# Kernel optimization log

Measured on AMD Instinct MI355X. Metric: run time of the kernel, lower is better.

The kernel has to match this reference:

```python
import jax, jax.numpy as jnp
import numpy as np

NUM_HEADS = 4
LN_EPS = 1e-5


def setup_inputs() -> dict:
    key = jax.random.key(0)
    ks = jax.random.split(key, 12)
    B, S, D = 8, 2048, 256
    Dh = D // NUM_HEADS
    s = 0.02
    return {
        "descriptors": jax.random.normal(ks[0], (B, S, D), jnp.float32),
        # cached rotary embedding (cos, sin) pair broadcastable over heads
        "keypoints": jax.random.normal(ks[1], (2, B, 1, S, Dh), jnp.float32),
        "Wqkv_w": jax.random.normal(ks[2], (3 * D, D), jnp.float32) * s,
        "Wqkv_b": jax.random.normal(ks[3], (3 * D,), jnp.float32) * s,
        "Wo_w": jax.random.normal(ks[4], (D, D), jnp.float32) * s,
        "Wo_b": jax.random.normal(ks[5], (D,), jnp.float32) * s,
        "W1_w": jax.random.normal(ks[6], (2 * D, 2 * D), jnp.float32) * s,
        "W1_b": jax.random.normal(ks[7], (2 * D,), jnp.float32) * s,
        "ln_g": jnp.ones((2 * D,), jnp.float32),
        "ln_b": jnp.zeros((2 * D,), jnp.float32),
        "W2_w": jax.random.normal(ks[8], (D, 2 * D), jnp.float32) * s,
        "W2_b": jax.random.normal(ks[9], (D,), jnp.float32) * s,
    }


def _rotate_half(x):
    # pairwise rotation: (x0,x1,x2,x3,...) -> (-x1,x0,-x3,x2,...)
    xr = x.reshape(x.shape[:-1] + (x.shape[-1] // 2, 2))
    return jnp.stack((-xr[..., 1], xr[..., 0]), axis=-1).reshape(x.shape)


def reference(descriptors, keypoints, Wqkv_w, Wqkv_b, Wo_w, Wo_b,
              W1_w, W1_b, ln_g, ln_b, W2_w, W2_b):
    B, S, D = descriptors.shape
    H = NUM_HEADS
    Dh = D // H
    # fused QKV projection; torch layout: last dim = (H, Dh, 3) interleaved
    qkv = descriptors @ Wqkv_w.T + Wqkv_b           # [B,S,3D]
    qkv = qkv.reshape(B, S, H, Dh, 3).transpose(0, 2, 1, 3, 4)  # [B,H,S,Dh,3]
    q, k, v = qkv[..., 0], qkv[..., 1], qkv[..., 2]
    # rotary embedding on q, k
    cos, sin = keypoints[0], keypoints[1]           # [B,1,S,Dh]
    q = q * cos + _rotate_half(q) * sin
    k = k * cos + _rotate_half(k) * sin
    # scaled dot-product attention
    scale = jnp.float32(Dh) ** -0.5
    sim = jnp.einsum('bhid,bhjd->bhij', q, k) * scale
    attn = jax.nn.softmax(sim, axis=-1)
    ctx = jnp.einsum('bhij,bhjd->bhid', attn, v)    # [B,H,S,Dh]
    ctx = ctx.transpose(0, 2, 1, 3).reshape(B, S, D)
    message = ctx @ Wo_w.T + Wo_b
    # FFN over concat(descriptors, message)
    x = jnp.concatenate([descriptors, message], axis=-1)  # [B,S,2D]
    x = x @ W1_w.T + W1_b
    mu = jnp.mean(x, axis=-1, keepdims=True)
    var = jnp.var(x, axis=-1, keepdims=True)
    x = (x - mu) * jax.lax.rsqrt(var + LN_EPS) * ln_g + ln_b
    x = jax.nn.gelu(x, approximate=False)
    x = x @ W2_w.T + W2_b
    return descriptors + x
```

## Files before the change

### kernel.cpp

```cpp
#include <hip/hip_runtime.h>
#include <math.h>

#define B_  8
#define S_  2048
#define D_  256
#define H_  4
#define DH  64
#define M_  (B_ * S_)
#define QS  4194304

typedef __attribute__((ext_vector_type(8))) short bf16x8;
typedef __attribute__((ext_vector_type(4))) float f32x4;
typedef unsigned short u16;
typedef unsigned int   u32;

#define AS1 __attribute__((address_space(1)))
#define AS3 __attribute__((address_space(3)))

__device__ __forceinline__ u16 f2bf(float x) {
    union { float f; u32 u; } c; c.f = x;
    u32 r = (c.u + 0x7fffu + ((c.u >> 16) & 1u)) >> 16;
    return (u16)r;
}
__device__ __forceinline__ float bf2f(u16 x) {
    union { u32 u; float f; } c; c.u = ((u32)x) << 16;
    return c.f;
}

__device__ __forceinline__ void gload16(const void* g, void* l) {
    __builtin_amdgcn_global_load_lds((const AS1 unsigned int*)g,
                                     (AS3 unsigned int*)l, 16, 0, 0);
}

__global__ __launch_bounds__(256) void cast7_kernel(
    const float* __restrict__ desc, u16* __restrict__ descb,
    const float* __restrict__ wqkv, u16* __restrict__ wqkvb,
    const float* __restrict__ wo,   const float* __restrict__ w1,
    u16* __restrict__ w1f,
    const float* __restrict__ w2,   u16* __restrict__ w2b,
    const float* __restrict__ w1_b, const float* __restrict__ wo_b,
    float* __restrict__ bias1f)
{
    int bid = blockIdx.x;
    const int tid = threadIdx.x;

    if (bid >= 5184) {
        const int row = bid - 5184;
        const int col = tid;
        const float* wrow = w1 + (size_t)row * 512 + 256;
        float acc = 0.f;
#pragma unroll 4
        for (int k = 0; k < 256; k++)
            acc += wrow[k] * wo[(size_t)k * 256 + col];
        w1f[(size_t)row * 512 + 256 + col] = f2bf(acc);
        return;
    }
    if (bid >= 4672) {
        __shared__ float red[4];
        const int n = bid - 4672;
        float p = w1[(size_t)n * 512 + 256 + tid] * wo_b[tid];
#pragma unroll
        for (int off = 1; off < 64; off <<= 1) p += __shfl_xor(p, off);
        if ((tid & 63) == 0) red[tid >> 6] = p;
        __syncthreads();
        if (tid == 0) bias1f[n] = red[0] + red[1] + red[2] + red[3] + w1_b[n];
        return;
    }
    if (bid >= 4544) {
        const int i = ((bid - 4544) * 256 + tid) * 4;
        const float4 v = *(const float4*)(w2 + i);
        u16 o[4] = {f2bf(v.x), f2bf(v.y), f2bf(v.z), f2bf(v.w)};
        *(uint2*)(w2b + i) = *(const uint2*)o;
        return;
    }
    if (bid >= 4288) {
        const int e = ((bid - 4288) * 256 + tid) * 4;
        const int row = e >> 9, col = e & 511;
        if (col < 256) {
            const float4 v = *(const float4*)(w1 + e);
            u16 o[4] = {f2bf(v.x), f2bf(v.y), f2bf(v.z), f2bf(v.w)};
            *(uint2*)(w1f + (size_t)row * 512 + col) = *(const uint2*)o;
        }
        return;
    }
    const float* s; u16* d;
    if (bid < 4096) { s = desc; d = descb; }
    else            { s = wqkv; d = wqkvb; bid -= 4096; }
    const int i = (bid * 256 + tid) * 4;
    const float4 v = *(const float4*)(s + i);
    u16 o[4] = {f2bf(v.x), f2bf(v.y), f2bf(v.z), f2bf(v.w)};
    *(uint2*)(d + i) = *(const uint2*)o;
}

template <int NT, int CONCAT, int RES, int OUTBF16>
__global__ __launch_bounds__(256) void gemm_bf16(
    const u16* __restrict__ A, const u16* __restrict__ A2,
    const u16* __restrict__ W, const float* __restrict__ bias,
    const float* __restrict__ res, float* __restrict__ Cf,
    u16* __restrict__ Cb, int K, int N, int ldc)
{
    __shared__ u16 As[128 * 64];
    __shared__ u16 Bs[NT * 32 * 64];
    const int tid  = threadIdx.x;
    const int w    = tid >> 6;
    const int lane = tid & 63;
    const int n    = lane & 15;
    const int quad = lane >> 4;
    const int m0   = blockIdx.x * 128;
    const int n0   = blockIdx.y * (NT * 32);
    const int m_off = (w >> 1) * 64;
    const int n_off = (w & 1) * (NT * 16);
    const int lrow = lane >> 3;
    const int lcol = (lane & 7) * 8;

    f32x4 acc[4][NT];
#pragma unroll
    for (int i = 0; i < 4; i++)
#pragma unroll
        for (int j = 0; j < NT; j++) acc[i][j] = (f32x4){0.f, 0.f, 0.f, 0.f};

    for (int k0 = 0; k0 < K; k0 += 64) {
        const u16* Asrc;
        int kb, lda;
        if (CONCAT) { Asrc = (k0 < 256) ? A : A2; kb = k0 & 255; lda = 256; }
        else        { Asrc = A; kb = k0; lda = K; }

        __syncthreads();
#pragma unroll
        for (int it = 0; it < 4; it++) {
            const int r0 = it * 32 + w * 8;
            gload16(Asrc + (size_t)(m0 + r0 + lrow) * lda + kb + lcol, &As[r0 * 64]);
        }
#pragma unroll
        for (int it = 0; it < NT; it++) {
            const int r0 = it * 32 + w * 8;
            gload16(W + (size_t)(n0 + r0 + lrow) * K + k0 + lcol, &Bs[r0 * 64]);
        }
        __syncthreads();

        bf16x8 af[4][2], bf[NT][2];
#pragma unroll
        for (int mt = 0; mt < 4; mt++)
#pragma unroll
            for (int t = 0; t < 2; t++)
                af[mt][t] = *(const bf16x8*)&As[(m_off + mt * 16 + n) * 64 + t * 32 + quad * 8];
#pragma unroll
        for (int nt = 0; nt < NT; nt++)
#pragma unroll
            for (int t = 0; t < 2; t++)
                bf[nt][t] = *(const bf16x8*)&Bs[(n_off + nt * 16 + n) * 64 + t * 32 + quad * 8];

#pragma unroll
        for (int mt = 0; mt < 4; mt++)
#pragma unroll
            for (int nt = 0; nt < NT; nt++) {
                acc[mt][nt] = __builtin_amdgcn_mfma_f32_16x16x32_bf16(af[mt][0], bf[nt][0], acc[mt][nt], 0, 0, 0);
                acc[mt][nt] = __builtin_amdgcn_mfma_f32_16x16x32_bf16(af[mt][1], bf[nt][1], acc[mt][nt], 0, 0, 0);
            }
    }

#pragma unroll
    for (int nt = 0; nt < NT; nt++) {
        const int col = n0 + n_off + nt * 16 + n;
        const float bv = bias[col];
#pragma unroll
        for (int mt = 0; mt < 4; mt++) {
#pragma unroll
            for (int r = 0; r < 4; r++) {
                const int row = m0 + m_off + mt * 16 + quad * 4 + r;
                float o = acc[mt][nt][r] + bv;
                if (RES) o += res[(size_t)row * ldc + col];
                if (OUTBF16) Cb[(size_t)row * ldc + col] = f2bf(o);
                else         Cf[(size_t)row * ldc + col] = o;
            }
        }
    }
}

#define QSCALE 0.18033688011112042f

__global__ __launch_bounds__(256) void ropevt_kernel(
    const u16* __restrict__ qkv, const float* __restrict__ kp,
    u16* __restrict__ q, u16* __restrict__ k, u16* __restrict__ vt)
{
    __shared__ u32 vbuf[32 * 128];

    const int bh = blockIdx.x;
    const int s0 = blockIdx.y * 128;
    const int b  = bh >> 2;
    const int h  = bh & 3;
    const int t  = threadIdx.x;
    const int dp = t & 31;
    const int d  = dp * 2;

    const size_t qkbase = ((size_t)bh * S_ + s0) * DH;
#pragma unroll
    for (int i = 0; i < 16; i++) {
        const int sl = i * 8 + (t >> 5);
        const int s  = s0 + sl;
        const u16* src = qkv + (size_t)(b * S_ + s) * 768 + h * 192 + dp * 6;
        const u32 w0 = *(const u32*)(src);
        const u32 w1 = *(const u32*)(src + 2);
        const u32 w2 = *(const u32*)(src + 4);
        const float qe = bf2f((u16)w0), ke = bf2f((u16)(w0 >> 16));
        const float qo = bf2f((u16)(w1 >> 16));
        const float ko = bf2f((u16)w2);

        const size_t kidx = ((size_t)b * S_ + s) * DH + d;
        const float2 cs = *(const float2*)(kp + kidx);
        const float2 sn = *(const float2*)(kp + (size_t)B_ * S_ * DH + kidx);

        const float qe2 = (qe * cs.x - qo * sn.x) * QSCALE;
        const float qo2 = (qo * cs.y + qe * sn.y) * QSCALE;
        const float ke2 = ke * cs.x - ko * sn.x;
        const float ko2 = ko * cs.y + ke * sn.y;

        const size_t oidx = qkbase + (size_t)sl * DH + d;
        *(u32*)(q + oidx) = (u32)f2bf(qe2) | ((u32)f2bf(qo2) << 16);
        *(u32*)(k + oidx) = (u32)f2bf(ke2) | ((u32)f2bf(ko2) << 16);
        vbuf[dp * 128 + (sl ^ dp)] = (w1 & 0xffffu) | (w2 & 0xffff0000u);
    }
    __syncthreads();

    u16* vtp = vt + (size_t)bh * DH * S_ + s0;
#pragma unroll
    for (int i = 0; i < 16; i++) {
        const int dd  = i * 4 + (t >> 6);
        const int sp  = t & 63;
        const int dpr = dd >> 1;
        const u32 a = vbuf[dpr * 128 + ((2 * sp)     ^ dpr)];
        const u32 c = vbuf[dpr * 128 + ((2 * sp + 1) ^ dpr)];
        const u32 o = (dd & 1) ? ((a >> 16)      | (c & 0xffff0000u))
                               : ((a & 0xffffu)  | (c << 16));
        *(u32*)(vtp + (size_t)dd * S_ + 2 * sp) = o;
    }
}

#define NEG12L2E -17.312340490667562f

__global__ __launch_bounds__(256, 2) void attn_kernel(
    const u16* __restrict__ q, const u16* __restrict__ k,
    const u16* __restrict__ vt, u16* __restrict__ ctx)
{
    __shared__ u16 ks[128 * 64];
    __shared__ u16 qs[128 * 64];
    __shared__ u16 vs[64 * 128];
    __shared__ u16 ps[128 * 128];

    const int tid  = threadIdx.x;
    const int w    = tid >> 6;
    const int lane = tid & 63;
    const int n    = lane & 15;
    const int quad = lane >> 4;
    const int lrow = lane >> 3;
    const int vrow = lane >> 4;
    const int bh   = blockIdx.x;
    const int q0   = blockIdx.y * 128;
    const int b    = bh >> 2;
    const int h    = bh & 3;
    const int nsw  = n & 7;

    const int kcol  = (((lane & 7) ^ lrow) * 8);
    const int vcol0 = (((lane & 15) ^ vrow) * 8);
    const int vcol1 = (((lane & 15) ^ (4 + vrow)) * 8);

    const u16* qbase = q  + (size_t)bh * S_ * DH;
    const u16* kbase = k  + (size_t)bh * S_ * DH;
    const u16* vbase = vt + (size_t)bh * DH * S_;

#pragma unroll
    for (int it = 0; it < 4; it++) {
        const int idx = it * 256 + tid;
        const int row = idx >> 3;
        const int c8  = idx & 7;
        *(uint4*)&qs[row * 64 + ((c8 ^ (row & 7)) * 8)] =
            *(const uint4*)(qbase + (size_t)(q0 + row) * DH + c8 * 8);
    }
    __syncthreads();

    bf16x8 qf[2][2];
#pragma unroll
    for (int mb = 0; mb < 2; mb++) {
        qf[mb][0] = *(const bf16x8*)&qs[(w * 32 + mb * 16 + n) * 64 + ((quad       ^ nsw) * 8)];
        qf[mb][1] = *(const bf16x8*)&qs[(w * 32 + mb * 16 + n) * 64 + (((4 + quad) ^ nsw) * 8)];
    }

    f32x4 o[2][4];
#pragma unroll
    for (int mb = 0; mb < 2; mb++)
#pragma unroll
        for (int j = 0; j < 4; j++) o[mb][j] = (f32x4){0.f, 0.f, 0.f, 0.f};
    float lrun[2] = {0.f, 0.f};

    for (int kb = 0; kb < S_ / 128; kb++) {
        const int k0 = kb * 128;
        __syncthreads();
#pragma unroll
        for (int it = 0; it < 4; it++) {
            const int r0 = w * 32 + it * 8;
            gload16(kbase + (size_t)(k0 + r0 + lrow) * DH + kcol, &ks[r0 * 64]);
            const int d0 = w * 16 + it * 4;
            gload16(vbase + (size_t)(d0 + vrow) * S_ + k0 + ((it & 1) ? vcol1 : vcol0),
                    &vs[d0 * 128]);
        }
        __syncthreads();

        f32x4 sacc[2][8];
#pragma unroll
        for (int mb = 0; mb < 2; mb++)
#pragma unroll
            for (int j = 0; j < 8; j++)
                sacc[mb][j] = (f32x4){NEG12L2E, NEG12L2E, NEG12L2E, NEG12L2E};
        __builtin_amdgcn_s_setprio(1);
#pragma unroll
        for (int t = 0; t < 2; t++) {
#pragma unroll
            for (int j = 0; j < 8; j++) {
                const bf16x8 kf = *(const bf16x8*)
                    &ks[(16 * j + n) * 64 + (((t * 4 + quad) ^ nsw) * 8)];
                sacc[0][j] = __builtin_amdgcn_mfma_f32_16x16x32_bf16(kf, qf[0][t], sacc[0][j], 0, 0, 0);
                sacc[1][j] = __builtin_amdgcn_mfma_f32_16x16x32_bf16(kf, qf[1][t], sacc[1][j], 0, 0, 0);
            }
        }
        __builtin_amdgcn_s_setprio(0);

#pragma unroll
        for (int mb = 0; mb < 2; mb++) {
            float rs = 0.f;
            const int prow = (w * 32 + mb * 16 + n) * 128;
#pragma unroll
            for (int j = 0; j < 8; j++) {
                const float e0 = __builtin_amdgcn_exp2f(sacc[mb][j][0]);
                const float e1 = __builtin_amdgcn_exp2f(sacc[mb][j][1]);
                const float e2 = __builtin_amdgcn_exp2f(sacc[mb][j][2]);
                const float e3 = __builtin_amdgcn_exp2f(sacc[mb][j][3]);
                rs += (e0 + e1) + (e2 + e3);
                uint2 pk;
                pk.x = (u32)f2bf(e0) | ((u32)f2bf(e1) << 16);
                pk.y = (u32)f2bf(e2) | ((u32)f2bf(e3) << 16);
                const int blk = (4 * j + quad) ^ (nsw << 2);
                *(uint2*)&ps[prow + blk * 4] = pk;
            }
            lrun[mb] += rs;
        }

        __builtin_amdgcn_s_setprio(1);
#pragma unroll
        for (int kt = 0; kt < 4; kt++) {
            const bf16x8 pf0 = *(const bf16x8*)
                &ps[(w * 32 +      n) * 128 + ((32 * kt + 8 * quad) ^ (nsw << 4))];
            const bf16x8 pf1 = *(const bf16x8*)
                &ps[(w * 32 + 16 + n) * 128 + ((32 * kt + 8 * quad) ^ (nsw << 4))];
#pragma unroll
            for (int nt = 0; nt < 4; nt++) {
                const bf16x8 vf = *(const bf16x8*)
                    &vs[(16 * nt + n) * 128 + (((kt * 4 + quad) ^ nsw) * 8)];
                o[0][nt] = __builtin_amdgcn_mfma_f32_16x16x32_bf16(pf0, vf, o[0][nt], 0, 0, 0);
                o[1][nt] = __builtin_amdgcn_mfma_f32_16x16x32_bf16(pf1, vf, o[1][nt], 0, 0, 0);
            }
        }
        __builtin_amdgcn_s_setprio(0);
    }

#pragma unroll
    for (int mb = 0; mb < 2; mb++) {
        float s = lrun[mb];
        s += __shfl_xor(s, 16);
        s += __shfl_xor(s, 32);
        lrun[mb] = s;
    }

#pragma unroll
    for (int mb = 0; mb < 2; mb++) {
#pragma unroll
        for (int r = 0; r < 4; r++) {
            const float sv = __shfl(lrun[mb], quad * 4 + r);
            const float inv = 1.f / sv;
            const int row = q0 + w * 32 + mb * 16 + quad * 4 + r;
#pragma unroll
            for (int nt = 0; nt < 4; nt++)
                ctx[((size_t)b * S_ + row) * D_ + h * DH + 16 * nt + n] = f2bf(o[mb][nt][r] * inv);
        }
    }
}

__global__ __launch_bounds__(256) void ln_gelu_kernel(
    const u16* __restrict__ x, const float* __restrict__ g,
    const float* __restrict__ bt, u16* __restrict__ y)
{
    const int m    = blockIdx.x * 4 + (threadIdx.x >> 6);
    const int lane = threadIdx.x & 63;
    const int c0   = lane * 8;
    uint4 xv = *(const uint4*)(x + (size_t)m * 512 + c0);
    const u16* xp = (const u16*)&xv;
    float v[8];
    float s = 0.f, sq = 0.f;
#pragma unroll
    for (int j = 0; j < 8; j++) {
        v[j] = bf2f(xp[j]);
        s  += v[j];
        sq += v[j] * v[j];
    }
#pragma unroll
    for (int off = 1; off < 64; off <<= 1) {
        s  += __shfl_xor(s, off);
        sq += __shfl_xor(sq, off);
    }
    const float mu   = s * (1.f / 512.f);
    const float var  = sq * (1.f / 512.f) - mu * mu;
    const float rstd = rsqrtf(var + 1e-5f);

    const float4 g0 = *(const float4*)(g  + c0);
    const float4 g1 = *(const float4*)(g  + c0 + 4);
    const float4 b0 = *(const float4*)(bt + c0);
    const float4 b1 = *(const float4*)(bt + c0 + 4);
    const float gg[8] = {g0.x, g0.y, g0.z, g0.w, g1.x, g1.y, g1.z, g1.w};
    const float bb[8] = {b0.x, b0.y, b0.z, b0.w, b1.x, b1.y, b1.z, b1.w};
    u16 o[8];
#pragma unroll
    for (int j = 0; j < 8; j++) {
        const float yj = (v[j] - mu) * rstd * gg[j] + bb[j];
        o[j] = f2bf(0.5f * yj * (1.f + erff(yj * 0.70710678118654752f)));
    }
    *(uint4*)(y + (size_t)m * 512 + c0) = *(const uint4*)o;
}

extern "C" void kernel_launch(void* const* d_in, const int* in_sizes, int n_in,
                              void* d_out, int out_size, void* d_ws, size_t ws_size,
                              hipStream_t stream)
{
    const float* desc   = (const float*)d_in[0];
    const float* kp     = (const float*)d_in[1];
    const float* Wqkv_w = (const float*)d_in[2];
    const float* Wqkv_b = (const float*)d_in[3];
    const float* Wo_w   = (const float*)d_in[4];
    const float* Wo_b   = (const float*)d_in[5];
    const float* W1_w   = (const float*)d_in[6];
    const float* W1_b   = (const float*)d_in[7];
    const float* ln_g   = (const float*)d_in[8];
    const float* ln_b   = (const float*)d_in[9];
    const float* W2_w   = (const float*)d_in[10];
    const float* W2_b   = (const float*)d_in[11];
    float* out = (float*)d_out;
    float* ws  = (float*)d_ws;

    u16*   qkvb  = (u16*)ws;
    u16*   x1b   = (u16*)(ws + 2 * (size_t)QS);
    u16*   qb    = (u16*)(ws + 3 * (size_t)QS);
    u16*   kb    = (u16*)(ws + (size_t)(3.5 * QS));
    u16*   x1g   = qb;
    u16*   ctxb  = (u16*)(ws + (size_t)(4.5 * QS));
    u16*   descb = (u16*)(ws + 5 * (size_t)QS);
    float* bias1f = ws + (size_t)(5.5 * QS);
    u16*   wpool = (u16*)(ws + 6 * (size_t)QS);
    u16*   vtb   = (u16*)(ws + (size_t)(6.5 * QS));
    u16* wqkvb = wpool;
    u16* w2b   = wqkvb + 196608;
    u16* w1f   = w2b   + 131072;

    const dim3 blk(256);

    cast7_kernel<<<dim3(5696), blk, 0, stream>>>(
        desc, descb, Wqkv_w, wqkvb, Wo_w, W1_w, w1f, W2_w, w2b,
        W1_b, Wo_b, bias1f);

    gemm_bf16<4, 0, 0, 1><<<dim3(M_ / 128, 768 / 128), blk, 0, stream>>>(
        descb, nullptr, wqkvb, Wqkv_b, nullptr, nullptr, qkvb, 256, 768, 768);

    ropevt_kernel<<<dim3(B_ * H_, S_ / 128), blk, 0, stream>>>(
        qkvb, kp, qb, kb, vtb);

    attn_kernel<<<dim3(B_ * H_, S_ / 128), blk, 0, stream>>>(qb, kb, vtb, ctxb);

    gemm_bf16<4, 1, 0, 1><<<dim3(M_ / 128, 512 / 128), blk, 0, stream>>>(
        descb, ctxb, w1f, bias1f, nullptr, nullptr, x1b, 512, 512, 512);

    ln_gelu_kernel<<<dim3(M_ / 4), blk, 0, stream>>>(x1b, ln_g, ln_b, x1g);

    gemm_bf16<2, 0, 1, 0><<<dim3(M_ / 128, 256 / 64), blk, 0, stream>>>(
        x1g, nullptr, w2b, W2_b, desc, out, nullptr, 512, 256, 256);
}
```

Baseline: 236.4 us.

## Fuse RoPE/V-transpose into attention kernel via cooperative grid sync

Merges the rotary-embedding/V-transpose kernel and the attention kernel into one cooperative launch. A grid-wide barrier separates the two phases, and shared memory is pooled so both phases fit in one allocation. Q fragments are now loaded straight from global memory into registers instead of being staged through LDS. This removes one kernel launch and its gap. The cost is a grid sync over 512 blocks, which needs every block resident at once (two per CU under the launch bounds), and the direct Q loads may be less coalesced.

Result: slower. 321.1 us (+35.8%).

```diff
diff --git a/kernel.cpp b/kernel.cpp
--- a/kernel.cpp
+++ b/kernel.cpp
@@ -1,4 +1,5 @@
 #include <hip/hip_runtime.h>
+#include <hip/hip_cooperative_groups.h>
 #include <math.h>
 
 #define B_  8
@@ -177,87 +178,83 @@
     }
 }
 
-#define QSCALE 0.18033688011112042f
-
-__global__ __launch_bounds__(256) void ropevt_kernel(
+#define QSCALE   0.18033688011112042f
+#define NEG12L2E -17.312340490667562f
+
+__global__ __launch_bounds__(256, 2) void ropeattn_kernel(
     const u16* __restrict__ qkv, const float* __restrict__ kp,
-    u16* __restrict__ q, u16* __restrict__ k, u16* __restrict__ vt)
+    u16* __restrict__ q, u16* __restrict__ k, u16* __restrict__ vt,
+    u16* __restrict__ ctx)
 {
-    __shared__ u32 vbuf[32 * 128];
-
-    const int bh = blockIdx.x;
-    const int s0 = blockIdx.y * 128;
-    const int b  = bh >> 2;
-    const int h  = bh & 3;
-    const int t  = threadIdx.x;
-    const int dp = t & 31;
-    const int d  = dp * 2;
-
-    const size_t qkbase = ((size_t)bh * S_ + s0) * DH;
-#pragma unroll
-    for (int i = 0; i < 16; i++) {
-        const int sl = i * 8 + (t >> 5);
-        const int s  = s0 + sl;
-        const u16* src = qkv + (size_t)(b * S_ + s) * 768 + h * 192 + dp * 6;
-        const u32 w0 = *(const u32*)(src);
-        const u32 w1 = *(const u32*)(src + 2);
-        const u32 w2 = *(const u32*)(src + 4);
-        const float qe = bf2f((u16)w0), ke = bf2f((u16)(w0 >> 16));
-        const float qo = bf2f((u16)(w1 >> 16));
-        const float ko = bf2f((u16)w2);
-
-        const size_t kidx = ((size_t)b * S_ + s) * DH + d;
-        const float2 cs = *(const float2*)(kp + kidx);
-        const float2 sn = *(const float2*)(kp + (size_t)B_ * S_ * DH + kidx);
-
-        const float qe2 = (qe * cs.x - qo * sn.x) * QSCALE;
-        const float qo2 = (qo * cs.y + qe * sn.y) * QSCALE;
-        const float ke2 = ke * cs.x - ko * sn.x;
-        const float ko2 = ko * cs.y + ke * sn.y;
-
-        const size_t oidx = qkbase + (size_t)sl * DH + d;
-        *(u32*)(q + oidx) = (u32)f2bf(qe2) | ((u32)f2bf(qo2) << 16);
-        *(u32*)(k + oidx) = (u32)f2bf(ke2) | ((u32)f2bf(ko2) << 16);
-        vbuf[dp * 128 + (sl ^ dp)] = (w1 & 0xffffu) | (w2 & 0xffff0000u);
-    }
-    __syncthreads();
-
-    u16* vtp = vt + (size_t)bh * DH * S_ + s0;
-#pragma unroll
-    for (int i = 0; i < 16; i++) {
-        const int dd  = i * 4 + (t >> 6);
-        const int sp  = t & 63;
-        const int dpr = dd >> 1;
-        const u32 a = vbuf[dpr * 128 + ((2 * sp)     ^ dpr)];
-        const u32 c = vbuf[dpr * 128 + ((2 * sp + 1) ^ dpr)];
-        const u32 o = (dd & 1) ? ((a >> 16)      | (c & 0xffff0000u))
-                               : ((a & 0xffffu)  | (c << 16));
-        *(u32*)(vtp + (size_t)dd * S_ + 2 * sp) = o;
-    }
-}
-
-#define NEG12L2E -17.312340490667562f
-
-__global__ __launch_bounds__(256, 2) void attn_kernel(
-    const u16* __restrict__ q, const u16* __restrict__ k,
-    const u16* __restrict__ vt, u16* __restrict__ ctx)
-{
-    __shared__ u16 ks[128 * 64];
-    __shared__ u16 qs[128 * 64];
-    __shared__ u16 vs[64 * 128];
-    __shared__ u16 ps[128 * 128];
+    __shared__ u16 pool[32768];
+    u16* ks = pool;
+    u16* vs = pool + 8192;
+    u16* ps = pool + 16384;
+    u32* vbuf = (u32*)pool;
 
     const int tid  = threadIdx.x;
+    const int bh   = blockIdx.x;
+    const int b    = bh >> 2;
+    const int h    = bh & 3;
+
+    {
+        const int s0 = blockIdx.y * 128;
+        const int t  = tid;
+        const int dp = t & 31;
+        const int d  = dp * 2;
+
+        const size_t qkbase = ((size_t)bh * S_ + s0) * DH;
+#pragma unroll
+        for (int i = 0; i < 16; i++) {
+            const int sl = i * 8 + (t >> 5);
+            const int s  = s0 + sl;
+            const u16* src = qkv + (size_t)(b * S_ + s) * 768 + h * 192 + dp * 6;
+            const u32 w0 = *(const u32*)(src);
+            const u32 w1 = *(const u32*)(src + 2);
+            const u32 w2 = *(const u32*)(src + 4);
+            const float qe = bf2f((u16)w0), ke = bf2f((u16)(w0 >> 16));
+            const float qo = bf2f((u16)(w1 >> 16));
+            const float ko = bf2f((u16)w2);
+
+            const size_t kidx = ((size_t)b * S_ + s) * DH + d;
+            const float2 cs = *(const float2*)(kp + kidx);
+            const float2 sn = *(const float2*)(kp + (size_t)B_ * S_ * DH + kidx);
+
+            const float qe2 = (qe * cs.x - qo * sn.x) * QSCALE;
+            const float qo2 = (qo * cs.y + qe * sn.y) * QSCALE;
+            const float ke2 = ke * cs.x - ko * sn.x;
+            const float ko2 = ko * cs.y + ke * sn.y;
+
+            const size_t oidx = qkbase + (size_t)sl * DH + d;
+            *(u32*)(q + oidx) = (u32)f2bf(qe2) | ((u32)f2bf(qo2) << 16);
+            *(u32*)(k + oidx) = (u32)f2bf(ke2) | ((u32)f2bf(ko2) << 16);
+            vbuf[dp * 128 + (sl ^ dp)] = (w1 & 0xffffu) | (w2 & 0xffff0000u);
+        }
+        __syncthreads();
+
+        u16* vtp = vt + (size_t)bh * DH * S_ + s0;
+#pragma unroll
+        for (int i = 0; i < 16; i++) {
+            const int dd  = i * 4 + (t >> 6);
+            const int sp  = t & 63;
+            const int dpr = dd >> 1;
+            const u32 a = vbuf[dpr * 128 + ((2 * sp)     ^ dpr)];
+            const u32 c = vbuf[dpr * 128 + ((2 * sp + 1) ^ dpr)];
+            const u32 o = (dd & 1) ? ((a >> 16)      | (c & 0xffff0000u))
+                                   : ((a & 0xffffu)  | (c << 16));
+            *(u32*)(vtp + (size_t)dd * S_ + 2 * sp) = o;
+        }
+    }
+
+    cooperative_groups::this_grid().sync();
+
     const int w    = tid >> 6;
     const int lane = tid & 63;
     const int n    = lane & 15;
     const int quad = lane >> 4;
     const int lrow = lane >> 3;
     const int vrow = lane >> 4;
-    const int bh   = blockIdx.x;
     const int q0   = blockIdx.y * 128;
-    const int b    = bh >> 2;
-    const int h    = bh & 3;
     const int nsw  = n & 7;
 
     const int kcol  = (((lane & 7) ^ lrow) * 8);
@@ -268,22 +265,13 @@
     const u16* kbase = k  + (size_t)bh * S_ * DH;
     const u16* vbase = vt + (size_t)bh * DH * S_;
 
-#pragma unroll
-    for (int it = 0; it < 4; it++) {
-        const int idx = it * 256 + tid;
-        const int row = idx >> 3;
-        const int c8  = idx & 7;
-        *(uint4*)&qs[row * 64 + ((c8 ^ (row & 7)) * 8)] =
-            *(const uint4*)(qbase + (size_t)(q0 + row) * DH + c8 * 8);
-    }
-    __syncthreads();
-
     bf16x8 qf[2][2];
 #pragma unroll
-    for (int mb = 0; mb < 2; mb++) {
-        qf[mb][0] = *(const bf16x8*)&qs[(w * 32 + mb * 16 + n) * 64 + ((quad       ^ nsw) * 8)];
-        qf[mb][1] = *(const bf16x8*)&qs[(w * 32 + mb * 16 + n) * 64 + (((4 + quad) ^ nsw) * 8)];
-    }
+    for (int mb = 0; mb < 2; mb++)
+#pragma unroll
+        for (int t = 0; t < 2; t++)
+            qf[mb][t] = *(const bf16x8*)(qbase +
+                (size_t)(q0 + w * 32 + mb * 16 + n) * DH + (t * 4 + quad) * 8);
 
     f32x4 o[2][4];
 #pragma unroll
@@ -467,10 +455,14 @@
     gemm_bf16<4, 0, 0, 1><<<dim3(M_ / 128, 768 / 128), blk, 0, stream>>>(
         descb, nullptr, wqkvb, Wqkv_b, nullptr, nullptr, qkvb, 256, 768, 768);
 
-    ropevt_kernel<<<dim3(B_ * H_, S_ / 128), blk, 0, stream>>>(
-        qkvb, kp, qb, kb, vtb);
-
-    attn_kernel<<<dim3(B_ * H_, S_ / 128), blk, 0, stream>>>(qb, kb, vtb, ctxb);
+    {
+        const u16* a0 = qkvb; const float* a1 = kp;
+        u16* a2 = qb; u16* a3 = kb; u16* a4 = vtb; u16* a5 = ctxb;
+        void* args[] = {(void*)&a0, (void*)&a1, (void*)&a2,
+                        (void*)&a3, (void*)&a4, (void*)&a5};
+        hipLaunchCooperativeKernel((void*)ropeattn_kernel,
+                                   dim3(B_ * H_, S_ / 128), blk, args, 0, stream);
+    }
 
     gemm_bf16<4, 1, 0, 1><<<dim3(M_ / 128, 512 / 128), blk, 0, stream>>>(
         descb, ctxb, w1f, bias1f, nullptr, nullptr, x1b, 512, 512, 512);
```
